# Kernel optimization log

Hardware: AMD Instinct MI355X
Metric: run time of the kernel (lower is better)

Reference implementation:

```python
import jax, jax.numpy as jnp
import numpy as np

WS = 8
NH = 6
LF_DIM = 64
HF_DIM = 192
HEAD_DIM = HF_DIM // NH


def _rpb_index(ws):
    # static numpy computation of the relative-position index, (N, N) int
    coords = np.stack(np.meshgrid(np.arange(ws), np.arange(ws), indexing='ij')).reshape(2, -1)
    rel = coords[:, :, None] - coords[:, None, :]          # (2, N, N)
    rel = rel.transpose(1, 2, 0).astype(np.int64)          # (N, N, 2)
    rel[..., 0] += ws - 1
    rel[..., 1] += ws - 1
    rel[..., 0] *= 2 * ws - 1
    return rel.sum(-1)                                     # (N, N)

_RPB_IDX = _rpb_index(WS)


def _layernorm(x, g, b, eps=1e-5):
    mu = jnp.mean(x, axis=-1, keepdims=True)
    var = jnp.mean(jnp.square(x - mu), axis=-1, keepdims=True)
    return (x - mu) * jax.lax.rsqrt(var + eps) * g + b


def _window_partition(x, ws):
    # (B, C, H, W) -> (B*nH*nW, ws*ws, C)
    B, C, H, W = x.shape
    x = x.reshape(B, C, H // ws, ws, W // ws, ws)
    x = x.transpose(0, 2, 4, 3, 5, 1)                      # B nH nW ws ws C
    return x.reshape(-1, ws * ws, C)


def _window_reverse(wins, ws, H, W):
    # (B*nH*nW, ws*ws, C) -> (B, C, H, W)
    nH, nW = H // ws, W // ws
    B = wins.shape[0] // (nH * nW)
    C = wins.shape[-1]
    x = wins.reshape(B, nH, nW, ws, ws, C)
    x = x.transpose(0, 5, 1, 3, 2, 4)                      # B C nH ws nW ws
    return x.reshape(B, C, H, W)


def setup_inputs() -> dict:
    key = jax.random.key(0)
    ks = jax.random.split(key, 16)
    B, H, W = 4, 256, 256
    s = 0.02
    return {
        'y_lf': jax.random.normal(ks[0], (B, LF_DIM, H, W), jnp.float32),
        'y_hf': jax.random.normal(ks[1], (B, HF_DIM, H, W), jnp.float32),
        'norm_lf_g': jnp.ones((LF_DIM,), jnp.float32),
        'norm_lf_b': jnp.zeros((LF_DIM,), jnp.float32),
        'norm_hf_g': jnp.ones((HF_DIM,), jnp.float32),
        'norm_hf_b': jnp.zeros((HF_DIM,), jnp.float32),
        'Wq': jax.random.normal(ks[2], (LF_DIM, HF_DIM), jnp.float32) * s,
        'bq': jnp.zeros((HF_DIM,), jnp.float32),
        'Wk': jax.random.normal(ks[3], (HF_DIM, HF_DIM), jnp.float32) * s,
        'bk': jnp.zeros((HF_DIM,), jnp.float32),
        'Wv': jax.random.normal(ks[4], (HF_DIM, HF_DIM), jnp.float32) * s,
        'bv': jnp.zeros((HF_DIM,), jnp.float32),
        'Wo': jax.random.normal(ks[5], (HF_DIM, HF_DIM), jnp.float32) * s,
        'bo': jnp.zeros((HF_DIM,), jnp.float32),
        'rpb_table': jax.random.normal(ks[6], ((2 * WS - 1) ** 2, NH), jnp.float32) * s,
    }


def reference(y_lf, y_hf, norm_lf_g, norm_lf_b, norm_hf_g, norm_hf_b,
              Wq, bq, Wk, bk, Wv, bv, Wo, bo, rpb_table):
    B, _, H, W = y_lf.shape
    ws, N = WS, WS * WS
    # H, W chosen divisible by ws so the reflect-pad in the original is a no-op
    lf_w = _window_partition(y_lf, ws)                     # (bw, N, C_lf)
    hf_w = _window_partition(y_hf, ws)                     # (bw, N, C_hf)
    hf_residual = hf_w
    lf_n = _layernorm(lf_w, norm_lf_g, norm_lf_b)
    hf_n = _layernorm(hf_w, norm_hf_g, norm_hf_b)
    bw = lf_w.shape[0]
    Q = (lf_n @ Wq + bq).reshape(bw, N, NH, HEAD_DIM).transpose(0, 2, 1, 3)
    K = (hf_n @ Wk + bk).reshape(bw, N, NH, HEAD_DIM).transpose(0, 2, 1, 3)
    V = (hf_n @ Wv + bv).reshape(bw, N, NH, HEAD_DIM).transpose(0, 2, 1, 3)
    scale = HEAD_DIM ** -0.5
    attn = jnp.einsum('bhnd,bhmd->bhnm', Q, K) * scale     # (bw, h, N, N)
    bias = rpb_table[_RPB_IDX.reshape(-1)].reshape(N, N, NH).transpose(2, 0, 1)
    attn = jax.nn.softmax(attn + bias[None], axis=-1)
    out = jnp.einsum('bhnm,bhmd->bhnd', attn, V)
    out = out.transpose(0, 2, 1, 3).reshape(bw, N, HF_DIM)
    out = out @ Wo + bo + hf_residual
    return _window_reverse(out, ws, H, W)                  # (B, C_hf, H, W)
```

## Files before the change

### kernel.cpp

```cpp
#include <hip/hip_runtime.h>
#include <cstdint>
#include <cstddef>

#define DEVI __device__ __forceinline__

typedef __bf16 bf16x8 __attribute__((ext_vector_type(8)));
typedef float  floatx4 __attribute__((ext_vector_type(4)));

constexpr int NHEAD = 6;
constexpr int CLF = 64, CHF = 192;
constexpr int IMG = 256;
constexpr int HW  = IMG * IMG;

constexpr int P_WQ  = 72;
constexpr int P_WKV = 200;
constexpr int P_WO  = 40;
constexpr int PQK = 40;
constexpr int PVT = 72;
constexpr int PP  = 72;

constexpr int OFF_WKV = 0;
constexpr int OFF_WO  = 25600;
constexpr int OFF_K   = 40960;
constexpr int OFF_VT  = 46080;
constexpr int OFF_P   = 50688;
constexpr int OFF_RED = 59904;
constexpr int SMEM_BYTES = 64000;

DEVI unsigned short f2b(float f) {
  unsigned u = __float_as_uint(f);
  u += 0x7fffu + ((u >> 16) & 1u);
  return (unsigned short)(u >> 16);
}
DEVI float b2f(unsigned short s) { return __uint_as_float(((unsigned)s) << 16); }

DEVI floatx4 mfma_bf16(bf16x8 a, bf16x8 b, floatx4 c) {
  return __builtin_amdgcn_mfma_f32_16x16x32_bf16(a, b, c, 0, 0, 0);
}

__global__ void wca_prep(const float* __restrict__ Wq, const float* __restrict__ Wk,
                         const float* __restrict__ Wv, const float* __restrict__ Wo,
                         unsigned short* __restrict__ wT) {
  int i = blockIdx.x * 256 + threadIdx.x;
  if (i < 12288) {
    int n = i >> 6, k = i & 63;
    wT[i] = f2b(Wq[k * 192 + n]);
  } else if (i < 49152) {
    int j = i - 12288, n = j / 192, k = j - n * 192;
    wT[i] = f2b(Wk[k * 192 + n]);
  } else if (i < 86016) {
    int j = i - 49152, n = j / 192, k = j - n * 192;
    wT[i] = f2b(Wv[k * 192 + n]);
  } else {
    int j = i - 86016, n = j / 192, k = j - n * 192;
    wT[i] = f2b(Wo[k * 192 + n]);
  }
}

__global__ __launch_bounds__(256, 2) void wca_main(
    const float* __restrict__ ylf, const float* __restrict__ yhf,
    const float* __restrict__ glf, const float* __restrict__ blf,
    const float* __restrict__ ghf, const float* __restrict__ bhf,
    const float* __restrict__ bq,  const float* __restrict__ bk,
    const float* __restrict__ bv,  const float* __restrict__ bo,
    const float* __restrict__ rpb, const unsigned short* __restrict__ wT,
    float* __restrict__ out) {
  __shared__ __align__(16) char smem[SMEM_BYTES];
  unsigned short* s_wkv = (unsigned short*)(smem + OFF_WKV);
  unsigned short* s_wq  = s_wkv;
  unsigned short* s_wo  = (unsigned short*)(smem + OFF_WO);
  unsigned short* s_k   = (unsigned short*)(smem + OFF_K);
  unsigned short* s_vt  = (unsigned short*)(smem + OFF_VT);
  unsigned short* s_lf  = (unsigned short*)(smem + OFF_P);
  unsigned short* s_p   = s_lf;
  float* s_red = (float*)(smem + OFF_RED);
  unsigned short* s_rpb = (unsigned short*)(smem + OFF_RED);

  const int tid  = threadIdx.x;
  const int lane = tid & 63;
  const int wv   = tid >> 6;
  const int quad = lane >> 4;
  const int l16  = lane & 15;

  const int g   = blockIdx.x;
  const int wid = ((g & 7) << 9) | (g >> 3);
  const int b   = wid >> 10;
  const int wy  = (wid >> 5) & 31;
  const int wx  = wid & 31;
  const int h0  = wy << 3, w0 = wx << 3;

  const int t_own = tid & 63;
  const int cg    = tid >> 6;
  const int ty    = t_own >> 3, tx = t_own & 7;

  float lfv[16], hfv[48];
  float ls = 0.f, l2 = 0.f, hs = 0.f, h2 = 0.f;
  {
    const float* p = ylf + ((size_t)(b * CLF + cg * 16) * IMG + (h0 + ty)) * IMG + (w0 + tx);
#pragma unroll
    for (int k = 0; k < 16; k++) {
      float v = p[(size_t)k * HW];
      lfv[k] = v; ls += v; l2 += v * v;
    }
  }
  {
    const float* p = yhf + ((size_t)(b * CHF + cg * 48) * IMG + (h0 + ty)) * IMG + (w0 + tx);
#pragma unroll
    for (int k = 0; k < 48; k++) {
      float v = p[(size_t)k * HW];
      hfv[k] = v; hs += v; h2 += v * v;
    }
  }
  s_red[0 * 256 + (cg << 6) + t_own] = ls;
  s_red[1 * 256 + (cg << 6) + t_own] = l2;
  s_red[2 * 256 + (cg << 6) + t_own] = hs;
  s_red[3 * 256 + (cg << 6) + t_own] = h2;
  __syncthreads();
  float su = 0.f, sq = 0.f, hu = 0.f, hq = 0.f;
#pragma unroll
  for (int gg = 0; gg < 4; gg++) {
    su += s_red[0 * 256 + (gg << 6) + t_own];
    sq += s_red[1 * 256 + (gg << 6) + t_own];
    hu += s_red[2 * 256 + (gg << 6) + t_own];
    hq += s_red[3 * 256 + (gg << 6) + t_own];
  }
  const float mu_lf = su * (1.f / 64.f);
  const float rs_lf = rsqrtf(sq * (1.f / 64.f) - mu_lf * mu_lf + 1e-5f);
  const float mu_hf = hu * (1.f / 192.f);
  const float rs_hf = rsqrtf(hq * (1.f / 192.f) - mu_hf * mu_hf + 1e-5f);

#pragma unroll
  for (int j = 0; j < 4; j++) {
    uint64_t w = 0;
#pragma unroll
    for (int m = 0; m < 4; m++) {
      int c = cg * 16 + j * 4 + m;
      float v = (lfv[j * 4 + m] - mu_lf) * rs_lf * glf[c] + blf[c];
      w |= (uint64_t)f2b(v) << (16 * m);
    }
    *(uint64_t*)(s_lf + t_own * PP + cg * 16 + j * 4) = w;
  }
#pragma unroll
  for (int j = 0; j < 12; j++) {
    uint64_t w = 0;
#pragma unroll
    for (int m = 0; m < 4; m++) {
      int c = cg * 48 + j * 4 + m;
      float v = (hfv[j * 4 + m] - mu_hf) * rs_hf * ghf[c] + bhf[c];
      w |= (uint64_t)f2b(v) << (16 * m);
    }
    *(uint64_t*)(s_wkv + t_own * P_WKV + cg * 48 + j * 4) = w;
  }
  __syncthreads();

  bf16x8 lfr0 = *(const bf16x8*)(s_lf + (wv * 16 + l16) * PP + quad * 8);
  bf16x8 lfr1 = *(const bf16x8*)(s_lf + (wv * 16 + l16) * PP + 32 + quad * 8);
  bf16x8 hfr[6];
#pragma unroll
  for (int ks = 0; ks < 6; ks++)
    hfr[ks] = *(const bf16x8*)(s_wkv + (wv * 16 + l16) * P_WKV + ks * 32 + quad * 8);
  __syncthreads();

  const unsigned short* wqT = wT;
  const unsigned short* wkT = wT + 12288;
  const unsigned short* wvT = wT + 49152;
  const unsigned short* woT = wT + 86016;

#pragma unroll
  for (int i = 0; i < 6; i++) {
    int p = i * 256 + tid;
    int n = p >> 3, sub = p & 7;
    *(uint4*)(s_wq + n * P_WQ + sub * 8) = *(const uint4*)(wqT + n * 64 + sub * 8);
  }
  for (int i = tid; i < 225 * NHEAD; i += 256) s_rpb[i] = f2b(rpb[i]);
  __syncthreads();

  const int rowbase = wv * 16 + quad * 4;

  bf16x8 aq[NHEAD];
#pragma unroll
  for (int h = 0; h < NHEAD; h++) {
#pragma unroll
    for (int nt = 0; nt < 2; nt++) {
      const int n = h * 32 + nt * 16 + l16;
      floatx4 acc = {0.f, 0.f, 0.f, 0.f};
      acc = mfma_bf16(lfr0, *(const bf16x8*)(s_wq + n * P_WQ + quad * 8), acc);
      acc = mfma_bf16(lfr1, *(const bf16x8*)(s_wq + n * P_WQ + 32 + quad * 8), acc);
      const float bqv = bq[n];
#pragma unroll
      for (int r = 0; r < 4; r++)
        s_p[(rowbase + r) * PP + nt * 16 + l16] = f2b(acc[r] + bqv);
    }
    aq[h] = *(const bf16x8*)(s_p + (wv * 16 + l16) * PP + quad * 8);
  }
  __syncthreads();

  auto stageKV = [&](int h) {
    const unsigned short* sk = wkT + h * 6144;
    const unsigned short* sv = wvT + h * 6144;
#pragma unroll
    for (int i = 0; i < 3; i++) {
      int p = i * 256 + tid;
      int nl = p / 24, sub = p - nl * 24;
      *(uint4*)(s_wkv + nl * P_WKV + sub * 8) = *(const uint4*)(sk + nl * 192 + sub * 8);
      *(uint4*)(s_wkv + (32 + nl) * P_WKV + sub * 8) = *(const uint4*)(sv + nl * 192 + sub * 8);
    }
  };

  stageKV(0);
  __syncthreads();

  floatx4 oa[12];
  const floatx4 zero = {0.f, 0.f, 0.f, 0.f};
#pragma unroll
  for (int ct = 0; ct < 12; ct++) oa[ct] = zero;

#pragma unroll
  for (int h = 0; h < NHEAD; h++) {
#pragma unroll
    for (int nt = 0; nt < 2; nt++) {
      const int n = h * 32 + nt * 16 + l16;
      const int nl = nt * 16 + l16;
      floatx4 acc = {0.f, 0.f, 0.f, 0.f};
#pragma unroll
      for (int ks = 0; ks < 6; ks++)
        acc = mfma_bf16(hfr[ks], *(const bf16x8*)(s_wkv + nl * P_WKV + ks * 32 + quad * 8), acc);
      const float bkv = bk[n];
#pragma unroll
      for (int r = 0; r < 4; r++)
        s_k[(rowbase + r) * PQK + nt * 16 + l16] = f2b(acc[r] + bkv);
    }
#pragma unroll
    for (int nt = 0; nt < 2; nt++) {
      const int n = h * 32 + nt * 16 + l16;
      const int nl = nt * 16 + l16;
      floatx4 acc = {0.f, 0.f, 0.f, 0.f};
#pragma unroll
      for (int ks = 0; ks < 6; ks++)
        acc = mfma_bf16(hfr[ks], *(const bf16x8*)(s_wkv + (32 + nl) * P_WKV + ks * 32 + quad * 8), acc);
      const float bvv = bv[n];
#pragma unroll
      for (int r = 0; r < 4; r++)
        s_vt[(nt * 16 + l16) * PVT + rowbase + r] = f2b(acc[r] + bvv);
    }
    __syncthreads();

#pragma unroll
    for (int i = 0; i < 3; i++) {
      int p = i * 256 + tid;
      int n = p >> 2, sub = p & 3;
      *(uint4*)(s_wo + n * P_WO + sub * 8) = *(const uint4*)(woT + n * 192 + h * 32 + sub * 8);
    }
    if (h + 1 < NHEAD) stageKV(h + 1);

    float sv[4][4];
#pragma unroll
    for (int ct = 0; ct < 4; ct++) {
      bf16x8 kb = *(const bf16x8*)(s_k + (ct * 16 + l16) * PQK + quad * 8);
      floatx4 acc = {0.f, 0.f, 0.f, 0.f};
      acc = mfma_bf16(aq[h], kb, acc);
#pragma unroll
      for (int r = 0; r < 4; r++) {
        int row = rowbase + r, col = ct * 16 + l16;
        int dy = (row >> 3) - (col >> 3) + 7;
        int dx = (row & 7) - (col & 7) + 7;
        sv[ct][r] = acc[r] * 0.17677669529663688f + b2f(s_rpb[(dy * 15 + dx) * NHEAD + h]);
      }
    }
#pragma unroll
    for (int r = 0; r < 4; r++) {
      float m = fmaxf(fmaxf(sv[0][r], sv[1][r]), fmaxf(sv[2][r], sv[3][r]));
      m = fmaxf(m, __shfl_xor(m, 1));
      m = fmaxf(m, __shfl_xor(m, 2));
      m = fmaxf(m, __shfl_xor(m, 4));
      m = fmaxf(m, __shfl_xor(m, 8));
      const float L2E = 1.4426950408889634f;
      float e0 = exp2f((sv[0][r] - m) * L2E);
      float e1 = exp2f((sv[1][r] - m) * L2E);
      float e2 = exp2f((sv[2][r] - m) * L2E);
      float e3 = exp2f((sv[3][r] - m) * L2E);
      float s = e0 + e1 + e2 + e3;
      s += __shfl_xor(s, 1);
      s += __shfl_xor(s, 2);
      s += __shfl_xor(s, 4);
      s += __shfl_xor(s, 8);
      float inv = 1.f / s;
      sv[0][r] = e0 * inv; sv[1][r] = e1 * inv; sv[2][r] = e2 * inv; sv[3][r] = e3 * inv;
    }
#pragma unroll
    for (int ct = 0; ct < 4; ct++)
#pragma unroll
      for (int r = 0; r < 4; r++)
        s_p[(rowbase + r) * PP + ct * 16 + l16] = f2b(sv[ct][r]);

    floatx4 pv0 = {0.f, 0.f, 0.f, 0.f}, pv1 = {0.f, 0.f, 0.f, 0.f};
#pragma unroll
    for (int ks = 0; ks < 2; ks++) {
      bf16x8 pa = *(const bf16x8*)(s_p + (wv * 16 + l16) * PP + ks * 32 + quad * 8);
      pv0 = mfma_bf16(pa, *(const bf16x8*)(s_vt + (0 * 16 + l16) * PVT + ks * 32 + quad * 8), pv0);
      pv1 = mfma_bf16(pa, *(const bf16x8*)(s_vt + (1 * 16 + l16) * PVT + ks * 32 + quad * 8), pv1);
    }
#pragma unroll
    for (int r = 0; r < 4; r++) {
      s_p[(rowbase + r) * PP + l16]      = f2b(pv0[r]);
      s_p[(rowbase + r) * PP + 16 + l16] = f2b(pv1[r]);
    }
    bf16x8 aoh = *(const bf16x8*)(s_p + (wv * 16 + l16) * PP + quad * 8);
    __syncthreads();

#pragma unroll
    for (int ct = 0; ct < 12; ct++) {
      bf16x8 bb = *(const bf16x8*)(s_wo + (ct * 16 + l16) * P_WO + quad * 8);
      oa[ct] = mfma_bf16(aoh, bb, oa[ct]);
    }
  }

#pragma unroll
  for (int ct = 0; ct < 12; ct++) {
    const int col = ct * 16 + l16;
    const float bov = bo[col];
#pragma unroll
    for (int r = 0; r < 4; r++)
      s_wkv[(rowbase + r) * P_WKV + col] = f2b(oa[ct][r] + bov);
  }
  __syncthreads();

#pragma unroll
  for (int k = 0; k < 12; k++) {
    int chunk = k * 256 + tid;
    int c   = chunk >> 4;
    int sub = chunk & 15;
    int yy  = sub >> 1;
    int x4  = (sub & 1) << 2;
    int t0  = (yy << 3) + x4;
    size_t gidx = ((size_t)(b * CHF + c) * IMG + (h0 + yy)) * IMG + w0 + x4;
    float4 res = *(const float4*)(yhf + gidx);
    float4 v;
    v.x = b2f(s_wkv[(t0 + 0) * P_WKV + c]) + res.x;
    v.y = b2f(s_wkv[(t0 + 1) * P_WKV + c]) + res.y;
    v.z = b2f(s_wkv[(t0 + 2) * P_WKV + c]) + res.z;
    v.w = b2f(s_wkv[(t0 + 3) * P_WKV + c]) + res.w;
    *(float4*)(out + gidx) = v;
  }
}

extern "C" void kernel_launch(void* const* d_in, const int* in_sizes, int n_in,
                              void* d_out, int out_size, void* d_ws, size_t ws_size,
                              hipStream_t stream) {
  const float* ylf = (const float*)d_in[0];
  const float* yhf = (const float*)d_in[1];
  const float* glf = (const float*)d_in[2];
  const float* blf = (const float*)d_in[3];
  const float* ghf = (const float*)d_in[4];
  const float* bhf = (const float*)d_in[5];
  const float* Wq  = (const float*)d_in[6];
  const float* bq  = (const float*)d_in[7];
  const float* Wk  = (const float*)d_in[8];
  const float* bk  = (const float*)d_in[9];
  const float* Wv  = (const float*)d_in[10];
  const float* bv  = (const float*)d_in[11];
  const float* Wo  = (const float*)d_in[12];
  const float* bo  = (const float*)d_in[13];
  const float* rpb = (const float*)d_in[14];
  unsigned short* wT = (unsigned short*)d_ws;

  wca_prep<<<480, 256, 0, stream>>>(Wq, Wk, Wv, Wo, wT);
  wca_main<<<4096, 256, 0, stream>>>(ylf, yhf, glf, blf, ghf, bhf,
                                     bq, bk, bv, bo, rpb, wT, (float*)d_out);
}
```

Before: 640.5 us.

## Process two windows per 512-thread block sharing staged K/V/Wq/Wo weights

Each block now handles two adjacent windows with 512 threads. The bf16 weight tiles (Wq, per-head Wk/Wv, Wo slices) and the bias table are staged into LDS once and shared by both windows, halving weight staging traffic and barriers per window. The hf-normalized tile and the output transpose are split into two half-channel passes so both windows fit in about 80KB of LDS. The cost is more __syncthreads over larger blocks, extra passes for the hf handoff and epilogue, and fewer resident blocks per CU.

```diff
diff --git a/kernel.cpp b/kernel.cpp
--- a/kernel.cpp
+++ b/kernel.cpp
@@ -15,17 +15,18 @@
 constexpr int P_WQ  = 72;
 constexpr int P_WKV = 200;
 constexpr int P_WO  = 40;
+constexpr int P_HFH = 104;
 constexpr int PQK = 40;
 constexpr int PVT = 72;
 constexpr int PP  = 72;
 
 constexpr int OFF_WKV = 0;
 constexpr int OFF_WO  = 25600;
-constexpr int OFF_K   = 40960;
-constexpr int OFF_VT  = 46080;
-constexpr int OFF_P   = 50688;
-constexpr int OFF_RED = 59904;
-constexpr int SMEM_BYTES = 64000;
+constexpr int OFF_K0  = 40960;
+constexpr int OFF_VT0 = 51200;
+constexpr int OFF_P0  = 60416;
+constexpr int OFF_RPB = 78848;
+constexpr int SMEM_BYTES = 81552;
 
 DEVI unsigned short f2b(float f) {
   unsigned u = __float_as_uint(f);
@@ -57,7 +58,7 @@
   }
 }
 
-__global__ __launch_bounds__(256, 2) void wca_main(
+__global__ __launch_bounds__(512, 4) void wca_main(
     const float* __restrict__ ylf, const float* __restrict__ yhf,
     const float* __restrict__ glf, const float* __restrict__ blf,
     const float* __restrict__ ghf, const float* __restrict__ bhf,
@@ -66,31 +67,36 @@
     const float* __restrict__ rpb, const unsigned short* __restrict__ wT,
     float* __restrict__ out) {
   __shared__ __align__(16) char smem[SMEM_BYTES];
+
+  const int tid  = threadIdx.x;
+  const int win  = tid >> 8;
+  const int t256 = tid & 255;
+  const int lane = tid & 63;
+  const int wvw  = (tid >> 6) & 3;
+  const int quad = lane >> 4;
+  const int l16  = lane & 15;
+
   unsigned short* s_wkv = (unsigned short*)(smem + OFF_WKV);
   unsigned short* s_wq  = s_wkv;
   unsigned short* s_wo  = (unsigned short*)(smem + OFF_WO);
-  unsigned short* s_k   = (unsigned short*)(smem + OFF_K);
-  unsigned short* s_vt  = (unsigned short*)(smem + OFF_VT);
-  unsigned short* s_lf  = (unsigned short*)(smem + OFF_P);
+  unsigned short* s_hfh = (unsigned short*)(smem + win * 13312);
+  unsigned short* s_k   = (unsigned short*)(smem + OFF_K0  + win * 5120);
+  unsigned short* s_vt  = (unsigned short*)(smem + OFF_VT0 + win * 4608);
+  unsigned short* s_lf  = (unsigned short*)(smem + OFF_P0  + win * 9216);
   unsigned short* s_p   = s_lf;
-  float* s_red = (float*)(smem + OFF_RED);
-  unsigned short* s_rpb = (unsigned short*)(smem + OFF_RED);
-
-  const int tid  = threadIdx.x;
-  const int lane = tid & 63;
-  const int wv   = tid >> 6;
-  const int quad = lane >> 4;
-  const int l16  = lane & 15;
-
-  const int g   = blockIdx.x;
-  const int wid = ((g & 7) << 9) | (g >> 3);
+  float* s_red = (float*)(smem + OFF_K0 + win * 5120);
+  unsigned short* s_rpb = (unsigned short*)(smem + OFF_RPB);
+
+  const int g      = blockIdx.x;
+  const int pairid = ((g & 7) << 8) | (g >> 3);
+  const int wid    = pairid * 2 + win;
   const int b   = wid >> 10;
   const int wy  = (wid >> 5) & 31;
   const int wx  = wid & 31;
   const int h0  = wy << 3, w0 = wx << 3;
 
   const int t_own = tid & 63;
-  const int cg    = tid >> 6;
+  const int cg    = (tid >> 6) & 3;
   const int ty    = t_own >> 3, tx = t_own & 7;
 
   float lfv[16], hfv[48];
@@ -140,25 +146,46 @@
     }
     *(uint64_t*)(s_lf + t_own * PP + cg * 16 + j * 4) = w;
   }
-#pragma unroll
-  for (int j = 0; j < 12; j++) {
-    uint64_t w = 0;
-#pragma unroll
-    for (int m = 0; m < 4; m++) {
-      int c = cg * 48 + j * 4 + m;
-      float v = (hfv[j * 4 + m] - mu_hf) * rs_hf * ghf[c] + bhf[c];
-      w |= (uint64_t)f2b(v) << (16 * m);
-    }
-    *(uint64_t*)(s_wkv + t_own * P_WKV + cg * 48 + j * 4) = w;
-  }
-  __syncthreads();
-
-  bf16x8 lfr0 = *(const bf16x8*)(s_lf + (wv * 16 + l16) * PP + quad * 8);
-  bf16x8 lfr1 = *(const bf16x8*)(s_lf + (wv * 16 + l16) * PP + 32 + quad * 8);
+  if (cg < 2) {
+#pragma unroll
+    for (int j = 0; j < 12; j++) {
+      uint64_t w = 0;
+#pragma unroll
+      for (int m = 0; m < 4; m++) {
+        int c = cg * 48 + j * 4 + m;
+        float v = (hfv[j * 4 + m] - mu_hf) * rs_hf * ghf[c] + bhf[c];
+        w |= (uint64_t)f2b(v) << (16 * m);
+      }
+      *(uint64_t*)(s_hfh + t_own * P_HFH + cg * 48 + j * 4) = w;
+    }
+  }
+  __syncthreads();
+
+  bf16x8 lfr0 = *(const bf16x8*)(s_lf + (wvw * 16 + l16) * PP + quad * 8);
+  bf16x8 lfr1 = *(const bf16x8*)(s_lf + (wvw * 16 + l16) * PP + 32 + quad * 8);
   bf16x8 hfr[6];
 #pragma unroll
-  for (int ks = 0; ks < 6; ks++)
-    hfr[ks] = *(const bf16x8*)(s_wkv + (wv * 16 + l16) * P_WKV + ks * 32 + quad * 8);
+  for (int ks = 0; ks < 3; ks++)
+    hfr[ks] = *(const bf16x8*)(s_hfh + (wvw * 16 + l16) * P_HFH + ks * 32 + quad * 8);
+  __syncthreads();
+
+  if (cg >= 2) {
+#pragma unroll
+    for (int j = 0; j < 12; j++) {
+      uint64_t w = 0;
+#pragma unroll
+      for (int m = 0; m < 4; m++) {
+        int c = cg * 48 + j * 4 + m;
+        float v = (hfv[j * 4 + m] - mu_hf) * rs_hf * ghf[c] + bhf[c];
+        w |= (uint64_t)f2b(v) << (16 * m);
+      }
+      *(uint64_t*)(s_hfh + t_own * P_HFH + (cg - 2) * 48 + j * 4) = w;
+    }
+  }
+  __syncthreads();
+#pragma unroll
+  for (int ks = 0; ks < 3; ks++)
+    hfr[3 + ks] = *(const bf16x8*)(s_hfh + (wvw * 16 + l16) * P_HFH + ks * 32 + quad * 8);
   __syncthreads();
 
   const unsigned short* wqT = wT;
@@ -167,15 +194,15 @@
   const unsigned short* woT = wT + 86016;
 
 #pragma unroll
-  for (int i = 0; i < 6; i++) {
-    int p = i * 256 + tid;
+  for (int i = 0; i < 3; i++) {
+    int p = i * 512 + tid;
     int n = p >> 3, sub = p & 7;
     *(uint4*)(s_wq + n * P_WQ + sub * 8) = *(const uint4*)(wqT + n * 64 + sub * 8);
   }
-  for (int i = tid; i < 225 * NHEAD; i += 256) s_rpb[i] = f2b(rpb[i]);
-  __syncthreads();
-
-  const int rowbase = wv * 16 + quad * 4;
+  for (int i = tid; i < 225 * NHEAD; i += 512) s_rpb[i] = f2b(rpb[i]);
+  __syncthreads();
+
+  const int rowbase = wvw * 16 + quad * 4;
 
   bf16x8 aq[NHEAD];
 #pragma unroll
@@ -191,7 +218,7 @@
       for (int r = 0; r < 4; r++)
         s_p[(rowbase + r) * PP + nt * 16 + l16] = f2b(acc[r] + bqv);
     }
-    aq[h] = *(const bf16x8*)(s_p + (wv * 16 + l16) * PP + quad * 8);
+    aq[h] = *(const bf16x8*)(s_p + (wvw * 16 + l16) * PP + quad * 8);
   }
   __syncthreads();
 
@@ -200,10 +227,15 @@
     const unsigned short* sv = wvT + h * 6144;
 #pragma unroll
     for (int i = 0; i < 3; i++) {
-      int p = i * 256 + tid;
-      int nl = p / 24, sub = p - nl * 24;
-      *(uint4*)(s_wkv + nl * P_WKV + sub * 8) = *(const uint4*)(sk + nl * 192 + sub * 8);
-      *(uint4*)(s_wkv + (32 + nl) * P_WKV + sub * 8) = *(const uint4*)(sv + nl * 192 + sub * 8);
+      int p = i * 512 + tid;
+      if (p < 768) {
+        int nl = p / 24, sub = p - nl * 24;
+        *(uint4*)(s_wkv + nl * P_WKV + sub * 8) = *(const uint4*)(sk + nl * 192 + sub * 8);
+      } else {
+        int q = p - 768;
+        int nl = q / 24, sub = q - nl * 24;
+        *(uint4*)(s_wkv + (32 + nl) * P_WKV + sub * 8) = *(const uint4*)(sv + nl * 192 + sub * 8);
+      }
     }
   };
 
@@ -246,10 +278,12 @@
     __syncthreads();
 
 #pragma unroll
-    for (int i = 0; i < 3; i++) {
-      int p = i * 256 + tid;
-      int n = p >> 2, sub = p & 3;
-      *(uint4*)(s_wo + n * P_WO + sub * 8) = *(const uint4*)(woT + n * 192 + h * 32 + sub * 8);
+    for (int i = 0; i < 2; i++) {
+      int p = i * 512 + tid;
+      if (p < 768) {
+        int n = p >> 2, sub = p & 3;
+        *(uint4*)(s_wo + n * P_WO + sub * 8) = *(const uint4*)(woT + n * 192 + h * 32 + sub * 8);
+      }
     }
     if (h + 1 < NHEAD) stageKV(h + 1);
 
@@ -296,7 +330,7 @@
     floatx4 pv0 = {0.f, 0.f, 0.f, 0.f}, pv1 = {0.f, 0.f, 0.f, 0.f};
 #pragma unroll
     for (int ks = 0; ks < 2; ks++) {
-      bf16x8 pa = *(const bf16x8*)(s_p + (wv * 16 + l16) * PP + ks * 32 + quad * 8);
+      bf16x8 pa = *(const bf16x8*)(s_p + (wvw * 16 + l16) * PP + ks * 32 + quad * 8);
       pv0 = mfma_bf16(pa, *(const bf16x8*)(s_vt + (0 * 16 + l16) * PVT + ks * 32 + quad * 8), pv0);
       pv1 = mfma_bf16(pa, *(const bf16x8*)(s_vt + (1 * 16 + l16) * PVT + ks * 32 + quad * 8), pv1);
     }
@@ -305,7 +339,7 @@
       s_p[(rowbase + r) * PP + l16]      = f2b(pv0[r]);
       s_p[(rowbase + r) * PP + 16 + l16] = f2b(pv1[r]);
     }
-    bf16x8 aoh = *(const bf16x8*)(s_p + (wv * 16 + l16) * PP + quad * 8);
+    bf16x8 aoh = *(const bf16x8*)(s_p + (wvw * 16 + l16) * PP + quad * 8);
     __syncthreads();
 
 #pragma unroll
@@ -314,33 +348,39 @@
       oa[ct] = mfma_bf16(aoh, bb, oa[ct]);
     }
   }
-
-#pragma unroll
-  for (int ct = 0; ct < 12; ct++) {
-    const int col = ct * 16 + l16;
-    const float bov = bo[col];
-#pragma unroll
-    for (int r = 0; r < 4; r++)
-      s_wkv[(rowbase + r) * P_WKV + col] = f2b(oa[ct][r] + bov);
-  }
-  __syncthreads();
-
-#pragma unroll
-  for (int k = 0; k < 12; k++) {
-    int chunk = k * 256 + tid;
-    int c   = chunk >> 4;
-    int sub = chunk & 15;
-    int yy  = sub >> 1;
-    int x4  = (sub & 1) << 2;
-    int t0  = (yy << 3) + x4;
-    size_t gidx = ((size_t)(b * CHF + c) * IMG + (h0 + yy)) * IMG + w0 + x4;
-    float4 res = *(const float4*)(yhf + gidx);
-    float4 v;
-    v.x = b2f(s_wkv[(t0 + 0) * P_WKV + c]) + res.x;
-    v.y = b2f(s_wkv[(t0 + 1) * P_WKV + c]) + res.y;
-    v.z = b2f(s_wkv[(t0 + 2) * P_WKV + c]) + res.z;
-    v.w = b2f(s_wkv[(t0 + 3) * P_WKV + c]) + res.w;
-    *(float4*)(out + gidx) = v;
+  __syncthreads();
+
+#pragma unroll
+  for (int pass = 0; pass < 2; pass++) {
+#pragma unroll
+    for (int ct6 = 0; ct6 < 6; ct6++) {
+      const int ct  = pass * 6 + ct6;
+      const int col = ct * 16 + l16;
+      const float bov = bo[col];
+#pragma unroll
+      for (int r = 0; r < 4; r++)
+        s_hfh[(rowbase + r) * P_HFH + (col - pass * 96)] = f2b(oa[ct][r] + bov);
+    }
+    __syncthreads();
+#pragma unroll
+    for (int k = 0; k < 6; k++) {
+      int chunk = k * 256 + t256;
+      int cl  = chunk >> 4;
+      int sub = chunk & 15;
+      int yy  = sub >> 1;
+      int x4  = (sub & 1) << 2;
+      int t0  = (yy << 3) + x4;
+      int c   = pass * 96 + cl;
+      size_t gidx = ((size_t)(b * CHF + c) * IMG + (h0 + yy)) * IMG + w0 + x4;
+      float4 res = *(const float4*)(yhf + gidx);
+      float4 v;
+      v.x = b2f(s_hfh[(t0 + 0) * P_HFH + cl]) + res.x;
+      v.y = b2f(s_hfh[(t0 + 1) * P_HFH + cl]) + res.y;
+      v.z = b2f(s_hfh[(t0 + 2) * P_HFH + cl]) + res.z;
+      v.w = b2f(s_hfh[(t0 + 3) * P_HFH + cl]) + res.w;
+      *(float4*)(out + gidx) = v;
+    }
+    __syncthreads();
   }
 }
 
@@ -365,6 +405,6 @@
   unsigned short* wT = (unsigned short*)d_ws;
 
   wca_prep<<<480, 256, 0, stream>>>(Wq, Wk, Wv, Wo, wT);
-  wca_main<<<4096, 256, 0, stream>>>(ylf, yhf, glf, blf, ghf, bhf,
+  wca_main<<<2048, 512, 0, stream>>>(ylf, yhf, glf, blf, ghf, bhf,
                                      bq, bk, bv, bo, rpb, wT, (float*)d_out);
 }
```

New measurement: 727.3 us. 13.6% more time.

## Shrink LDS footprint with XOR swizzle and per-head RPB staging for 3 blocks/CU

Applied to the files above, without the earlier changes.

Removes row padding from the shared-memory tiles (K/V weights, P, V^T, Wo, K) and uses an XOR swizzle to avoid bank conflicts. The full relative-position-bias table is no longer staged up front; instead a double-buffered per-head slice is loaded alongside the next head's K/V weights. Shared memory use drops from 64000 to 54272 bytes and launch bounds are raised to 3 blocks per CU to increase occupancy. The higher occupancy target also caps registers per thread, which could cause spills given the large accumulator arrays.

```diff
diff --git a/kernel.cpp b/kernel.cpp
--- a/kernel.cpp
+++ b/kernel.cpp
@@ -12,20 +12,19 @@
 constexpr int IMG = 256;
 constexpr int HW  = IMG * IMG;
 
-constexpr int P_WQ  = 72;
-constexpr int P_WKV = 200;
-constexpr int P_WO  = 40;
-constexpr int PQK = 40;
-constexpr int PVT = 72;
-constexpr int PP  = 72;
-
 constexpr int OFF_WKV = 0;
-constexpr int OFF_WO  = 25600;
-constexpr int OFF_K   = 40960;
-constexpr int OFF_VT  = 46080;
-constexpr int OFF_P   = 50688;
-constexpr int OFF_RED = 59904;
-constexpr int SMEM_BYTES = 64000;
+constexpr int OFF_WO  = 24576;
+constexpr int OFF_K   = 36864;
+constexpr int OFF_VT  = 40960;
+constexpr int OFF_P   = 45056;
+constexpr int OFF_RPB = 53248;
+constexpr int SMEM_BYTES = 54272;
+
+constexpr int LOFF_HF  = 0;
+constexpr int LOFF_LF  = 25600;
+constexpr int LOFF_RED = 34816;
+constexpr int P_HFL = 200, P_LFL = 72;
+constexpr int P_WQ = 72;
 
 DEVI unsigned short f2b(float f) {
   unsigned u = __float_as_uint(f);
@@ -37,6 +36,8 @@
 DEVI floatx4 mfma_bf16(bf16x8 a, bf16x8 b, floatx4 c) {
   return __builtin_amdgcn_mfma_f32_16x16x32_bf16(a, b, c, 0, 0, 0);
 }
+
+DEVI int swz8(int row, int off) { return off ^ ((row & 7) << 3); }
 
 __global__ void wca_prep(const float* __restrict__ Wq, const float* __restrict__ Wk,
                          const float* __restrict__ Wv, const float* __restrict__ Wo,
@@ -57,7 +58,7 @@
   }
 }
 
-__global__ __launch_bounds__(256, 2) void wca_main(
+__global__ __launch_bounds__(256, 3) void wca_main(
     const float* __restrict__ ylf, const float* __restrict__ yhf,
     const float* __restrict__ glf, const float* __restrict__ blf,
     const float* __restrict__ ghf, const float* __restrict__ bhf,
@@ -66,15 +67,16 @@
     const float* __restrict__ rpb, const unsigned short* __restrict__ wT,
     float* __restrict__ out) {
   __shared__ __align__(16) char smem[SMEM_BYTES];
-  unsigned short* s_wkv = (unsigned short*)(smem + OFF_WKV);
-  unsigned short* s_wq  = s_wkv;
-  unsigned short* s_wo  = (unsigned short*)(smem + OFF_WO);
-  unsigned short* s_k   = (unsigned short*)(smem + OFF_K);
-  unsigned short* s_vt  = (unsigned short*)(smem + OFF_VT);
-  unsigned short* s_lf  = (unsigned short*)(smem + OFF_P);
-  unsigned short* s_p   = s_lf;
-  float* s_red = (float*)(smem + OFF_RED);
-  unsigned short* s_rpb = (unsigned short*)(smem + OFF_RED);
+  unsigned short* s_wkv  = (unsigned short*)(smem + OFF_WKV);
+  unsigned short* s_wo   = (unsigned short*)(smem + OFF_WO);
+  unsigned short* s_k    = (unsigned short*)(smem + OFF_K);
+  unsigned short* s_vt   = (unsigned short*)(smem + OFF_VT);
+  unsigned short* s_p    = (unsigned short*)(smem + OFF_P);
+  unsigned short* s_rpbh = (unsigned short*)(smem + OFF_RPB);
+  unsigned short* s_hfL = (unsigned short*)(smem + LOFF_HF);
+  unsigned short* s_lfL = (unsigned short*)(smem + LOFF_LF);
+  float* s_red = (float*)(smem + LOFF_RED);
+  unsigned short* s_wq = (unsigned short*)(smem);
 
   const int tid  = threadIdx.x;
   const int lane = tid & 63;
@@ -138,7 +140,7 @@
       float v = (lfv[j * 4 + m] - mu_lf) * rs_lf * glf[c] + blf[c];
       w |= (uint64_t)f2b(v) << (16 * m);
     }
-    *(uint64_t*)(s_lf + t_own * PP + cg * 16 + j * 4) = w;
+    *(uint64_t*)(s_lfL + t_own * P_LFL + cg * 16 + j * 4) = w;
   }
 #pragma unroll
   for (int j = 0; j < 12; j++) {
@@ -149,16 +151,16 @@
       float v = (hfv[j * 4 + m] - mu_hf) * rs_hf * ghf[c] + bhf[c];
       w |= (uint64_t)f2b(v) << (16 * m);
     }
-    *(uint64_t*)(s_wkv + t_own * P_WKV + cg * 48 + j * 4) = w;
-  }
-  __syncthreads();
-
-  bf16x8 lfr0 = *(const bf16x8*)(s_lf + (wv * 16 + l16) * PP + quad * 8);
-  bf16x8 lfr1 = *(const bf16x8*)(s_lf + (wv * 16 + l16) * PP + 32 + quad * 8);
+    *(uint64_t*)(s_hfL + t_own * P_HFL + cg * 48 + j * 4) = w;
+  }
+  __syncthreads();
+
+  bf16x8 lfr0 = *(const bf16x8*)(s_lfL + (wv * 16 + l16) * P_LFL + quad * 8);
+  bf16x8 lfr1 = *(const bf16x8*)(s_lfL + (wv * 16 + l16) * P_LFL + 32 + quad * 8);
   bf16x8 hfr[6];
 #pragma unroll
   for (int ks = 0; ks < 6; ks++)
-    hfr[ks] = *(const bf16x8*)(s_wkv + (wv * 16 + l16) * P_WKV + ks * 32 + quad * 8);
+    hfr[ks] = *(const bf16x8*)(s_hfL + (wv * 16 + l16) * P_HFL + ks * 32 + quad * 8);
   __syncthreads();
 
   const unsigned short* wqT = wT;
@@ -172,7 +174,6 @@
     int n = p >> 3, sub = p & 7;
     *(uint4*)(s_wq + n * P_WQ + sub * 8) = *(const uint4*)(wqT + n * 64 + sub * 8);
   }
-  for (int i = tid; i < 225 * NHEAD; i += 256) s_rpb[i] = f2b(rpb[i]);
   __syncthreads();
 
   const int rowbase = wv * 16 + quad * 4;
@@ -189,9 +190,9 @@
       const float bqv = bq[n];
 #pragma unroll
       for (int r = 0; r < 4; r++)
-        s_p[(rowbase + r) * PP + nt * 16 + l16] = f2b(acc[r] + bqv);
-    }
-    aq[h] = *(const bf16x8*)(s_p + (wv * 16 + l16) * PP + quad * 8);
+        s_p[(rowbase + r) * 64 + swz8(rowbase + r, nt * 16 + l16)] = f2b(acc[r] + bqv);
+    }
+    aq[h] = *(const bf16x8*)(s_p + (wv * 16 + l16) * 64 + swz8(wv * 16 + l16, quad * 8));
   }
   __syncthreads();
 
@@ -202,12 +203,18 @@
     for (int i = 0; i < 3; i++) {
       int p = i * 256 + tid;
       int nl = p / 24, sub = p - nl * 24;
-      *(uint4*)(s_wkv + nl * P_WKV + sub * 8) = *(const uint4*)(sk + nl * 192 + sub * 8);
-      *(uint4*)(s_wkv + (32 + nl) * P_WKV + sub * 8) = *(const uint4*)(sv + nl * 192 + sub * 8);
+      *(uint4*)(s_wkv + nl * 192 + swz8(nl, sub * 8)) =
+          *(const uint4*)(sk + nl * 192 + sub * 8);
+      *(uint4*)(s_wkv + (32 + nl) * 192 + swz8(32 + nl, sub * 8)) =
+          *(const uint4*)(sv + nl * 192 + sub * 8);
     }
   };
+  auto stageRPB = [&](int h) {
+    if (tid < 225) s_rpbh[(h & 1) * 256 + tid] = f2b(rpb[tid * 6 + h]);
+  };
 
   stageKV(0);
+  stageRPB(0);
   __syncthreads();
 
   floatx4 oa[12];
@@ -224,11 +231,12 @@
       floatx4 acc = {0.f, 0.f, 0.f, 0.f};
 #pragma unroll
       for (int ks = 0; ks < 6; ks++)
-        acc = mfma_bf16(hfr[ks], *(const bf16x8*)(s_wkv + nl * P_WKV + ks * 32 + quad * 8), acc);
+        acc = mfma_bf16(hfr[ks],
+            *(const bf16x8*)(s_wkv + nl * 192 + swz8(nl, ks * 32 + quad * 8)), acc);
       const float bkv = bk[n];
 #pragma unroll
       for (int r = 0; r < 4; r++)
-        s_k[(rowbase + r) * PQK + nt * 16 + l16] = f2b(acc[r] + bkv);
+        s_k[(rowbase + r) * 32 + nt * 16 + l16] = f2b(acc[r] + bkv);
     }
 #pragma unroll
     for (int nt = 0; nt < 2; nt++) {
@@ -237,11 +245,12 @@
       floatx4 acc = {0.f, 0.f, 0.f, 0.f};
 #pragma unroll
       for (int ks = 0; ks < 6; ks++)
-        acc = mfma_bf16(hfr[ks], *(const bf16x8*)(s_wkv + (32 + nl) * P_WKV + ks * 32 + quad * 8), acc);
+        acc = mfma_bf16(hfr[ks],
+            *(const bf16x8*)(s_wkv + (32 + nl) * 192 + swz8(32 + nl, ks * 32 + quad * 8)), acc);
       const float bvv = bv[n];
 #pragma unroll
       for (int r = 0; r < 4; r++)
-        s_vt[(nt * 16 + l16) * PVT + rowbase + r] = f2b(acc[r] + bvv);
+        s_vt[nl * 64 + swz8(nl, rowbase + r)] = f2b(acc[r] + bvv);
     }
     __syncthreads();
 
@@ -249,14 +258,14 @@
     for (int i = 0; i < 3; i++) {
       int p = i * 256 + tid;
       int n = p >> 2, sub = p & 3;
-      *(uint4*)(s_wo + n * P_WO + sub * 8) = *(const uint4*)(woT + n * 192 + h * 32 + sub * 8);
-    }
-    if (h + 1 < NHEAD) stageKV(h + 1);
+      *(uint4*)(s_wo + n * 32 + sub * 8) = *(const uint4*)(woT + n * 192 + h * 32 + sub * 8);
+    }
+    if (h + 1 < NHEAD) { stageKV(h + 1); stageRPB(h + 1); }
 
     float sv[4][4];
 #pragma unroll
     for (int ct = 0; ct < 4; ct++) {
-      bf16x8 kb = *(const bf16x8*)(s_k + (ct * 16 + l16) * PQK + quad * 8);
+      bf16x8 kb = *(const bf16x8*)(s_k + (ct * 16 + l16) * 32 + quad * 8);
       floatx4 acc = {0.f, 0.f, 0.f, 0.f};
       acc = mfma_bf16(aq[h], kb, acc);
 #pragma unroll
@@ -264,7 +273,7 @@
         int row = rowbase + r, col = ct * 16 + l16;
         int dy = (row >> 3) - (col >> 3) + 7;
         int dx = (row & 7) - (col & 7) + 7;
-        sv[ct][r] = acc[r] * 0.17677669529663688f + b2f(s_rpb[(dy * 15 + dx) * NHEAD + h]);
+        sv[ct][r] = acc[r] * 0.17677669529663688f + b2f(s_rpbh[(h & 1) * 256 + dy * 15 + dx]);
       }
     }
 #pragma unroll
@@ -291,37 +300,39 @@
     for (int ct = 0; ct < 4; ct++)
 #pragma unroll
       for (int r = 0; r < 4; r++)
-        s_p[(rowbase + r) * PP + ct * 16 + l16] = f2b(sv[ct][r]);
+        s_p[(rowbase + r) * 64 + swz8(rowbase + r, ct * 16 + l16)] = f2b(sv[ct][r]);
 
     floatx4 pv0 = {0.f, 0.f, 0.f, 0.f}, pv1 = {0.f, 0.f, 0.f, 0.f};
 #pragma unroll
     for (int ks = 0; ks < 2; ks++) {
-      bf16x8 pa = *(const bf16x8*)(s_p + (wv * 16 + l16) * PP + ks * 32 + quad * 8);
-      pv0 = mfma_bf16(pa, *(const bf16x8*)(s_vt + (0 * 16 + l16) * PVT + ks * 32 + quad * 8), pv0);
-      pv1 = mfma_bf16(pa, *(const bf16x8*)(s_vt + (1 * 16 + l16) * PVT + ks * 32 + quad * 8), pv1);
+      bf16x8 pa = *(const bf16x8*)(s_p + (wv * 16 + l16) * 64 + swz8(wv * 16 + l16, ks * 32 + quad * 8));
+      pv0 = mfma_bf16(pa, *(const bf16x8*)(s_vt + (0 * 16 + l16) * 64 + swz8(0 * 16 + l16, ks * 32 + quad * 8)), pv0);
+      pv1 = mfma_bf16(pa, *(const bf16x8*)(s_vt + (1 * 16 + l16) * 64 + swz8(1 * 16 + l16, ks * 32 + quad * 8)), pv1);
     }
 #pragma unroll
     for (int r = 0; r < 4; r++) {
-      s_p[(rowbase + r) * PP + l16]      = f2b(pv0[r]);
-      s_p[(rowbase + r) * PP + 16 + l16] = f2b(pv1[r]);
-    }
-    bf16x8 aoh = *(const bf16x8*)(s_p + (wv * 16 + l16) * PP + quad * 8);
+      s_p[(rowbase + r) * 64 + swz8(rowbase + r, l16)]      = f2b(pv0[r]);
+      s_p[(rowbase + r) * 64 + swz8(rowbase + r, 16 + l16)] = f2b(pv1[r]);
+    }
+    bf16x8 aoh = *(const bf16x8*)(s_p + (wv * 16 + l16) * 64 + swz8(wv * 16 + l16, quad * 8));
     __syncthreads();
 
 #pragma unroll
     for (int ct = 0; ct < 12; ct++) {
-      bf16x8 bb = *(const bf16x8*)(s_wo + (ct * 16 + l16) * P_WO + quad * 8);
+      bf16x8 bb = *(const bf16x8*)(s_wo + (ct * 16 + l16) * 32 + quad * 8);
       oa[ct] = mfma_bf16(aoh, bb, oa[ct]);
     }
   }
-
+  __syncthreads();
+
+  unsigned short* s_ostg = (unsigned short*)(smem);
 #pragma unroll
   for (int ct = 0; ct < 12; ct++) {
     const int col = ct * 16 + l16;
     const float bov = bo[col];
 #pragma unroll
     for (int r = 0; r < 4; r++)
-      s_wkv[(rowbase + r) * P_WKV + col] = f2b(oa[ct][r] + bov);
+      s_ostg[(rowbase + r) * 200 + col] = f2b(oa[ct][r] + bov);
   }
   __syncthreads();
 
@@ -336,10 +347,10 @@
     size_t gidx = ((size_t)(b * CHF + c) * IMG + (h0 + yy)) * IMG + w0 + x4;
     float4 res = *(const float4*)(yhf + gidx);
     float4 v;
-    v.x = b2f(s_wkv[(t0 + 0) * P_WKV + c]) + res.x;
-    v.y = b2f(s_wkv[(t0 + 1) * P_WKV + c]) + res.y;
-    v.z = b2f(s_wkv[(t0 + 2) * P_WKV + c]) + res.z;
-    v.w = b2f(s_wkv[(t0 + 3) * P_WKV + c]) + res.w;
+    v.x = b2f(s_ostg[(t0 + 0) * 200 + c]) + res.x;
+    v.y = b2f(s_ostg[(t0 + 1) * 200 + c]) + res.y;
+    v.z = b2f(s_ostg[(t0 + 2) * 200 + c]) + res.z;
+    v.w = b2f(s_ostg[(t0 + 3) * 200 + c]) + res.w;
     *(float4*)(out + gidx) = v;
   }
 }
```

Measured after the change: 844.3 us. 31.8% more time.
